# Optimization experiments

Measured on AMD Instinct MI355X. Metric: run time of the kernel, lower is better.

Reference implementation:

```python
import jax, jax.numpy as jnp
import numpy as np
from jax import lax

B, H, W = 256, 26, 4
LAT, QOUT = 64, 1024
K, D, Z = 4, 32, 64   # num_flows, num_ortho_vecs, z_size
STEPS = 100
BN_EPS = 1e-5


def setup_inputs():
    ks = iter(jax.random.split(jax.random.key(0), 80))
    def rn(shape, s=0.05):
        return jax.random.normal(next(ks), shape, jnp.float32) * s
    z1 = lambda n: jnp.zeros((n,), jnp.float32)
    o1 = lambda n: jnp.ones((n,), jnp.float32)
    return {
        "x": jax.random.normal(next(ks), (B, 1, H, W), jnp.float32),
        "eps": jax.random.normal(next(ks), (B, LAT), jnp.float32),
        "cw1": rn((32, 1, 3, 4)), "cb1": z1(32), "g1": o1(32), "be1": z1(32),
        "cw2": rn((16, 32, 5, 1)), "cb2": z1(16), "g2": o1(16), "be2": z1(16),
        "cw3": rn((8, 16, 7, 1)), "cb3": z1(8), "g3": o1(8), "be3": z1(8),
        "d1_w": rn((112, QOUT)), "d1_b": z1(QOUT), "bn1_g": o1(QOUT), "bn1_b": z1(QOUT),
        "mu_w": rn((QOUT, LAT)), "mu_b": z1(LAT),
        "lv_w": rn((QOUT, LAT)), "lv_b": z1(LAT),
        "ad_w": rn((QOUT, K * D * D)), "ad_b": z1(K * D * D),
        "adg1_w": rn((QOUT, K * D)), "adg1_b": z1(K * D),
        "adg2_w": rn((QOUT, K * D)), "adg2_b": z1(K * D),
        "aq_w": rn((QOUT, K * Z * D)), "aq_b": rn((K * Z * D,), 0.05),
        "ab_w": rn((QOUT, K * D)), "ab_b": z1(K * D),
        "d3_w": rn((LAT, QOUT)), "d3_b": z1(QOUT), "bn3_g": o1(QOUT), "bn3_b": z1(QOUT),
        "d4_w": rn((QOUT, 112)), "d4_b": z1(112), "bn4_g": o1(112), "bn4_b": z1(112),
        "tw1": rn((8, 16, 7, 1)), "tb1": z1(16), "tg1": o1(16), "tbe1": z1(16),
        "tw2": rn((16, 32, 5, 1)), "tb2": z1(32), "tg2": o1(32), "tbe2": z1(32),
        "tw3": rn((32, 1, 3, 4)), "tb3": z1(1),
    }


def _conv(x, w, b):
    y = lax.conv_general_dilated(x, w, (1, 1), 'VALID',
                                 dimension_numbers=('NCHW', 'OIHW', 'NCHW'))
    return y + b[None, :, None, None]


def _tconv(x, w, b):
    # torch ConvTranspose2d weight layout (in, out, kH, kW) == OIHW of the
    # forward conv being transposed -> transpose_kernel=True matches torch.
    y = lax.conv_transpose(x, w, (1, 1), 'VALID',
                           dimension_numbers=('NCHW', 'OIHW', 'NCHW'),
                           transpose_kernel=True)
    return y + b[None, :, None, None]


def _bn2d(x, g, b):  # BatchNorm2d, training mode (biased batch stats)
    m = x.mean((0, 2, 3), keepdims=True)
    v = ((x - m) ** 2).mean((0, 2, 3), keepdims=True)
    return (x - m) * lax.rsqrt(v + BN_EPS) * g[None, :, None, None] + b[None, :, None, None]


def _bn1d(x, g, b):  # BatchNorm1d, training mode
    m = x.mean(0)
    v = ((x - m) ** 2).mean(0)
    return (x - m) * lax.rsqrt(v + BN_EPS) * g + b


def reference(x, eps, cw1, cb1, g1, be1, cw2, cb2, g2, be2, cw3, cb3, g3, be3,
              d1_w, d1_b, bn1_g, bn1_b, mu_w, mu_b, lv_w, lv_b,
              ad_w, ad_b, adg1_w, adg1_b, adg2_w, adg2_b, aq_w, aq_b, ab_w, ab_b,
              d3_w, d3_b, bn3_g, bn3_b, d4_w, d4_b, bn4_g, bn4_b,
              tw1, tb1, tg1, tbe1, tw2, tb2, tg2, tbe2, tw3, tb3):
    # ---- encoder CNN ----
    h = jax.nn.relu(_bn2d(_conv(x, cw1, cb1), g1, be1))
    h = jax.nn.relu(_bn2d(_conv(h, cw2, cb2), g2, be2))
    h = jax.nn.relu(_bn2d(_conv(h, cw3, cb3), g3, be3))   # (B,8,14,1)
    out = h.reshape(B, -1)                                 # (B,112)
    out = jax.nn.relu(_bn1d(out @ d1_w + d1_b, bn1_g, bn1_b))
    mean = out @ mu_w + mu_b
    logvar = out @ lv_w + lv_b
    # ---- amortized flow parameters ----
    full_d = (out @ ad_w + ad_b).reshape(B, D, D, K)
    diag1 = jnp.tanh(out @ adg1_w + adg1_b).reshape(B, D, K)
    diag2 = jnp.tanh(out @ adg2_w + adg2_b).reshape(B, D, K)
    triu = jnp.triu(jnp.ones((D, D), x.dtype), 1)[None, :, :, None]
    di = jnp.arange(D)
    r1 = (full_d * triu).at[:, di, di, :].set(diag1)
    r2 = (jnp.transpose(full_d, (0, 2, 1, 3)) * triu).at[:, di, di, :].set(diag2)
    q = out @ aq_w + aq_b                                  # (B, K*Z*D)
    bflow = (out @ ab_w + ab_b).reshape(B, 1, D, K)
    # ---- Bjorck orthogonalization (100 fixed-point steps) ----
    qn = q.reshape(B * K, Z * D)
    qn = qn / jnp.linalg.norm(qn, axis=1, keepdims=True)
    amat = qn.reshape(B * K, Z, D)
    eye = jnp.eye(D, dtype=x.dtype)
    @jax.checkpoint
    def step(a, _):
        gram = jnp.einsum('nzd,nze->nde', a, a)            # a^T a, (N,D,D)
        a = jnp.einsum('nzd,nde->nze', a, eye + 0.5 * (eye - gram))
        return a, None
    amat, _ = lax.scan(step, amat, None, length=STEPS)
    q_ortho = amat.reshape(B, K, Z, D).transpose(1, 0, 2, 3)  # (K,B,Z,D)
    # ---- reparameterize + Sylvester flows ----
    z0 = mean + eps * jnp.exp(0.5 * logvar)
    z = z0
    ldj = jnp.zeros((B,), x.dtype)
    for k in range(K):
        r1k, r2k, qk, bk = r1[..., k], r2[..., k], q_ortho[k], bflow[..., k]
        qr2 = jnp.einsum('bzd,bed->bze', qk, r2k)          # q @ r2^T (B,Z,D)
        qr1 = jnp.einsum('bzd,bde->bze', qk, r1k)          # q @ r1   (B,Z,D)
        r2qzb = jnp.einsum('bz,bzd->bd', z, qr2)[:, None, :] + bk  # (B,1,D)
        z = jnp.einsum('bod,bzd->boz', jnp.tanh(r2qzb), qr1)[:, 0, :] + z
        dr1 = r1k[:, di, di]
        dr2 = r2k[:, di, di]
        diag_j = (1.0 - jnp.tanh(r2qzb) ** 2)[:, 0, :] * (dr1 * dr2) + 1.0
        ldj = ldj + jnp.log(jnp.abs(diag_j)).sum(-1)
    # ---- decoder ----
    d = jax.nn.relu(_bn1d(z @ d3_w + d3_b, bn3_g, bn3_b))
    d = jax.nn.relu(_bn1d(d @ d4_w + d4_b, bn4_g, bn4_b))
    d = d.reshape(B, 8, 14, 1)
    d = jax.nn.relu(_bn2d(_tconv(d, tw1, tb1), tg1, tbe1))
    d = jax.nn.relu(_bn2d(_tconv(d, tw2, tb2), tg2, tbe2))
    x_dec = _tconv(d, tw3, tb3)
    return (x_dec, mean, logvar, ldj, z0, z)
```

## Files before the change

kernel.cpp:

```cpp
#include <hip/hip_runtime.h>
#include <math.h>

#define NS_STEPS 30

typedef __attribute__((ext_vector_type(8))) _Float16 half8;
typedef __attribute__((ext_vector_type(4))) _Float16 half4v;
typedef __attribute__((ext_vector_type(8))) short short8;
typedef __attribute__((ext_vector_type(4))) float floatx4;

static __device__ inline unsigned short f2bf(float f) {
  union { float f; unsigned u; } v; v.f = f;
  unsigned r = v.u + 0x7fffu + ((v.u >> 16) & 1u);
  return (unsigned short)(r >> 16);
}
static __device__ inline float bf2f(unsigned short h) {
  union { unsigned u; float f; } v; v.u = ((unsigned)h) << 16;
  return v.f;
}

__global__ __launch_bounds__(256) void conv1_k(const float* __restrict__ x,
    const float* __restrict__ w, const float* __restrict__ bias,
    float* __restrict__ out) {
  __shared__ float ws[384];
  int tid = threadIdx.x;
  for (int i = tid; i < 384; i += 256) ws[i] = w[i];
  __syncthreads();
  int idx = blockIdx.x * 256 + tid;
  if (idx >= 196608) return;
  int b = idx / 768, r = idx % 768;
  int c = r / 24, h = r % 24;
  const float* xb = x + b * 104 + h * 4;
  const float* wc = ws + c * 12;
  float acc = bias[c];
  #pragma unroll
  for (int kh = 0; kh < 3; kh++) {
    #pragma unroll
    for (int kw = 0; kw < 4; kw++)
      acc += xb[kh * 4 + kw] * wc[kh * 4 + kw];
  }
  out[idx] = acc;
}

__global__ __launch_bounds__(256) void conv2_k(const float* __restrict__ in,
    const float* __restrict__ w, const float* __restrict__ bias,
    float* __restrict__ out) {
  __shared__ float ws[2560];
  int tid = threadIdx.x;
  for (int i = tid; i < 2560; i += 256) ws[i] = w[i];
  __syncthreads();
  int idx = blockIdx.x * 256 + tid;
  if (idx >= 81920) return;
  int b = idx / 320, r = idx % 320;
  int c = r / 20, h = r % 20;
  const float* ib = in + b * 768 + h;
  const float* wc = ws + c * 160;
  float acc = bias[c];
  for (int i = 0; i < 32; i++) {
    #pragma unroll
    for (int kh = 0; kh < 5; kh++)
      acc += ib[i * 24 + kh] * wc[i * 5 + kh];
  }
  out[idx] = acc;
}

__global__ __launch_bounds__(256) void conv3_k(const float* __restrict__ in,
    const float* __restrict__ w, const float* __restrict__ bias,
    float* __restrict__ out) {
  __shared__ float ws[896];
  int tid = threadIdx.x;
  for (int i = tid; i < 896; i += 256) ws[i] = w[i];
  __syncthreads();
  int idx = blockIdx.x * 256 + tid;
  if (idx >= 28672) return;
  int b = idx / 112, r = idx % 112;
  int c = r / 14, h = r % 14;
  const float* ib = in + b * 320 + h;
  const float* wc = ws + c * 112;
  float acc = bias[c];
  for (int i = 0; i < 16; i++) {
    #pragma unroll
    for (int kh = 0; kh < 7; kh++)
      acc += ib[i * 20 + kh] * wc[i * 7 + kh];
  }
  out[idx] = acc;
}

__global__ __launch_bounds__(256) void tconv1_k(const float* __restrict__ in,
    const float* __restrict__ w, const float* __restrict__ bias,
    float* __restrict__ out) {
  __shared__ float ws[896];
  int tid = threadIdx.x;
  for (int i = tid; i < 896; i += 256) ws[i] = w[i];
  __syncthreads();
  int idx = blockIdx.x * 256 + tid;
  if (idx >= 81920) return;
  int b = idx / 320, r = idx % 320;
  int c = r / 20, s = r % 20;
  float acc = bias[c];
  for (int o = 0; o < 8; o++) {
    #pragma unroll
    for (int kh = 0; kh < 7; kh++) {
      int hs = s - kh;
      if (hs >= 0 && hs < 14)
        acc += in[b * 112 + o * 14 + hs] * ws[o * 112 + c * 7 + kh];
    }
  }
  out[idx] = acc;
}

__global__ __launch_bounds__(256) void tconv2_k(const float* __restrict__ in,
    const float* __restrict__ w, const float* __restrict__ bias,
    float* __restrict__ out) {
  __shared__ float ws[2560];
  int tid = threadIdx.x;
  for (int i = tid; i < 2560; i += 256) ws[i] = w[i];
  __syncthreads();
  int idx = blockIdx.x * 256 + tid;
  if (idx >= 196608) return;
  int b = idx / 768, r = idx % 768;
  int c = r / 24, s = r % 24;
  float acc = bias[c];
  for (int o = 0; o < 16; o++) {
    #pragma unroll
    for (int kh = 0; kh < 5; kh++) {
      int hs = s - kh;
      if (hs >= 0 && hs < 20)
        acc += in[b * 320 + o * 20 + hs] * ws[o * 160 + c * 5 + kh];
    }
  }
  out[idx] = acc;
}

__global__ __launch_bounds__(256) void tconv3_k(const float* __restrict__ in,
    const float* __restrict__ w, const float* __restrict__ bias,
    float* __restrict__ out) {
  __shared__ float ws[384];
  int tid = threadIdx.x;
  for (int i = tid; i < 384; i += 256) ws[i] = w[i];
  __syncthreads();
  int idx = blockIdx.x * 256 + tid;
  if (idx >= 26624) return;
  int b = idx / 104, r = idx % 104;
  int sh = r / 4, sw = r % 4;
  float acc = bias[0];
  for (int o = 0; o < 32; o++) {
    #pragma unroll
    for (int kh = 0; kh < 3; kh++) {
      int hs = sh - kh;
      if (hs >= 0 && hs < 24)
        acc += in[b * 768 + o * 24 + hs] * ws[o * 12 + kh * 4 + sw];
    }
  }
  out[idx] = acc;
}

__global__ __launch_bounds__(256) void bn2d_k(float* __restrict__ x,
    const float* __restrict__ g, const float* __restrict__ be,
    int C, int HW) {
  __shared__ float rs[256], rs2[256];
  int c = blockIdx.x, tid = threadIdx.x;
  int total = 256 * HW;
  float s = 0.f, s2 = 0.f;
  for (int i = tid; i < total; i += 256) {
    int b = i / HW, j = i - b * HW;
    float v = x[(b * C + c) * HW + j];
    s += v; s2 += v * v;
  }
  rs[tid] = s; rs2[tid] = s2;
  __syncthreads();
  for (int off = 128; off > 0; off >>= 1) {
    if (tid < off) { rs[tid] += rs[tid + off]; rs2[tid] += rs2[tid + off]; }
    __syncthreads();
  }
  float m = rs[0] / (float)total;
  float var = rs2[0] / (float)total - m * m;
  float rstd = rsqrtf(var + 1e-5f) * g[c];
  float bb = be[c];
  for (int i = tid; i < total; i += 256) {
    int b = i / HW, j = i - b * HW;
    size_t idx = (size_t)(b * C + c) * HW + j;
    float v = (x[idx] - m) * rstd + bb;
    x[idx] = v > 0.f ? v : 0.f;
  }
}

__global__ __launch_bounds__(256) void bn1d_k(float* __restrict__ x,
    const float* __restrict__ g, const float* __restrict__ be, int N) {
  __shared__ float p1[8][32], p2[8][32];
  int t = threadIdx.x;
  int cl = t & 31, rg = t >> 5;
  int c = blockIdx.x * 32 + cl;
  float s = 0.f, s2 = 0.f;
  if (c < N) {
    for (int r = rg * 32; r < rg * 32 + 32; r++) {
      float v = x[r * N + c];
      s += v; s2 += v * v;
    }
  }
  p1[rg][cl] = s; p2[rg][cl] = s2;
  __syncthreads();
  float ts = 0.f, ts2 = 0.f;
  #pragma unroll
  for (int i = 0; i < 8; i++) { ts += p1[i][cl]; ts2 += p2[i][cl]; }
  float m = ts * (1.f / 256.f);
  float var = ts2 * (1.f / 256.f) - m * m;
  float rstd = rsqrtf(var + 1e-5f) * ((c < N) ? g[c] : 1.f);
  float bb = (c < N) ? be[c] : 0.f;
  if (c < N) {
    for (int r = rg * 32; r < rg * 32 + 32; r++) {
      float v = (x[r * N + c] - m) * rstd + bb;
      x[r * N + c] = v > 0.f ? v : 0.f;
    }
  }
}

__global__ __launch_bounds__(256) void gemm_os_k(const float* __restrict__ A,
    const float* __restrict__ W, const float* __restrict__ bias,
    float* __restrict__ C, int K, int N) {
  __shared__ float As[112 * 68];
  __shared__ float Bs[112 * 68];
  int tid = threadIdx.x;
  int nb = blockIdx.x, mb = blockIdx.y;
  int K16 = K >> 4;
  {
    int row = tid >> 2;
    const float* Ar = A + (size_t)(mb * 64 + row) * K;
    for (int i = 0; i < K16; i++) {
      int j = (tid & 3) + 4 * i;
      float4 v = *(const float4*)(Ar + j * 4);
      int k = j * 4;
      As[k * 68 + row] = v.x;
      As[(k + 1) * 68 + row] = v.y;
      As[(k + 2) * 68 + row] = v.z;
      As[(k + 3) * 68 + row] = v.w;
    }
  }
  {
    int n4 = (tid & 15) * 4;
    for (int i = 0; i < K16; i++) {
      int k = (tid >> 4) + 16 * i;
      float4 v = *(const float4*)(W + (size_t)k * N + nb * 64 + n4);
      *(float4*)(Bs + k * 68 + n4) = v;
    }
  }
  __syncthreads();
  int tm = tid >> 4, tn = tid & 15;
  int m0 = tm * 4, n0 = tn * 4;
  float acc[4][4] = {{0.f}};
  #pragma unroll 8
  for (int kk = 0; kk < K; kk++) {
    float4 a = *(const float4*)(As + kk * 68 + m0);
    float4 b = *(const float4*)(Bs + kk * 68 + n0);
    acc[0][0] += a.x*b.x; acc[0][1] += a.x*b.y; acc[0][2] += a.x*b.z; acc[0][3] += a.x*b.w;
    acc[1][0] += a.y*b.x; acc[1][1] += a.y*b.y; acc[1][2] += a.y*b.z; acc[1][3] += a.y*b.w;
    acc[2][0] += a.z*b.x; acc[2][1] += a.z*b.y; acc[2][2] += a.z*b.z; acc[2][3] += a.z*b.w;
    acc[3][0] += a.w*b.x; acc[3][1] += a.w*b.y; acc[3][2] += a.w*b.z; acc[3][3] += a.w*b.w;
  }
  #pragma unroll
  for (int i = 0; i < 4; i++) {
    int m = mb * 64 + m0 + i;
    #pragma unroll
    for (int j = 0; j < 4; j++) {
      int n = nb * 64 + n0 + j;
      C[(size_t)m * N + n] = acc[i][j] + bias[n];
    }
  }
}

__global__ __launch_bounds__(256) void gemm_ks_k(const float* __restrict__ A,
    const float* __restrict__ W, const float* __restrict__ bias,
    float* __restrict__ C) {
  __shared__ float As[64 * 68];
  __shared__ float Bs[64 * 68];
  int tid = threadIdx.x;
  int nb = blockIdx.x, mb = blockIdx.y, kc = blockIdx.z;
  int k0 = kc * 64;
  {
    int row = tid >> 2;
    const float* Ar = A + (size_t)(mb * 64 + row) * 1024 + k0;
    #pragma unroll
    for (int i = 0; i < 4; i++) {
      int j = (tid & 3) + 4 * i;
      float4 v = *(const float4*)(Ar + j * 4);
      int k = j * 4;
      As[k * 68 + row] = v.x;
      As[(k + 1) * 68 + row] = v.y;
      As[(k + 2) * 68 + row] = v.z;
      As[(k + 3) * 68 + row] = v.w;
    }
  }
  {
    int n4 = (tid & 15) * 4;
    int nbase = nb * 64 + n4;
    #pragma unroll
    for (int i = 0; i < 4; i++) {
      int k = (tid >> 4) + 16 * i;
      const float* Wr = W + (size_t)(k0 + k) * 112;
      float4 v;
      v.x = (nbase     < 112) ? Wr[nbase]     : 0.f;
      v.y = (nbase + 1 < 112) ? Wr[nbase + 1] : 0.f;
      v.z = (nbase + 2 < 112) ? Wr[nbase + 2] : 0.f;
      v.w = (nbase + 3 < 112) ? Wr[nbase + 3] : 0.f;
      *(float4*)(Bs + k * 68 + n4) = v;
    }
  }
  __syncthreads();
  int tm = tid >> 4, tn = tid & 15;
  int m0 = tm * 4, n0 = tn * 4;
  float acc[4][4] = {{0.f}};
  #pragma unroll 8
  for (int kk = 0; kk < 64; kk++) {
    float4 a = *(const float4*)(As + kk * 68 + m0);
    float4 b = *(const float4*)(Bs + kk * 68 + n0);
    acc[0][0] += a.x*b.x; acc[0][1] += a.x*b.y; acc[0][2] += a.x*b.z; acc[0][3] += a.x*b.w;
    acc[1][0] += a.y*b.x; acc[1][1] += a.y*b.y; acc[1][2] += a.y*b.z; acc[1][3] += a.y*b.w;
    acc[2][0] += a.z*b.x; acc[2][1] += a.z*b.y; acc[2][2] += a.z*b.z; acc[2][3] += a.z*b.w;
    acc[3][0] += a.w*b.x; acc[3][1] += a.w*b.y; acc[3][2] += a.w*b.z; acc[3][3] += a.w*b.w;
  }
  #pragma unroll
  for (int i = 0; i < 4; i++) {
    int m = mb * 64 + m0 + i;
    #pragma unroll
    for (int j = 0; j < 4; j++) {
      int n = nb * 64 + n0 + j;
      if (n < 112) {
        float v = acc[i][j] + (kc == 0 ? bias[n] : 0.f);
        atomicAdd(&C[m * 112 + n], v);
      }
    }
  }
}

__global__ __launch_bounds__(256) void prep_a_k(const float* __restrict__ A,
    short* __restrict__ ahi, short* __restrict__ alo) {
  int gi = blockIdx.x * 256 + threadIdx.x;
  int lane = gi & 63;
  int t = gi >> 6;
  int mt = t & 3; t >>= 2;
  int c = t & 31; int mb = t >> 5;
  int row = mb * 64 + mt * 16 + (lane & 15);
  int k0 = c * 32 + (lane >> 4) * 8;
  const float* src = A + (size_t)row * 1024 + k0;
  float4 v0 = *(const float4*)(src);
  float4 v1 = *(const float4*)(src + 4);
  float av[8] = {v0.x, v0.y, v0.z, v0.w, v1.x, v1.y, v1.z, v1.w};
  short8 h, lo;
  #pragma unroll
  for (int i = 0; i < 8; i++) {
    unsigned short hh = f2bf(av[i]);
    h[i] = (short)hh;
    lo[i] = (short)f2bf(av[i] - bf2f(hh));
  }
  *(short8*)(ahi + (size_t)gi * 8) = h;
  *(short8*)(alo + (size_t)gi * 8) = lo;
}

struct HeadArgs {
  const float* W[7];
  const float* b[7];
  float* dst[7];
  int off[8];
  int ldw[7];
  int op[7];
};

__global__ __launch_bounds__(256) void heads_mfma_k(const short* __restrict__ ahi,
                                                    const short* __restrict__ alo,
                                                    HeadArgs ha) {
  int tid = threadIdx.x;
  int nb = blockIdx.x;
  int gc = nb * 16;
  int r = 0;
  while (gc >= ha.off[r + 1]) r++;
  const float* Wp = ha.W[r];
  const float* bias = ha.b[r];
  float* dst = ha.dst[r];
  int ldw = ha.ldw[r];
  int op = ha.op[r];
  int nloc = gc - ha.off[r];

  int w = tid >> 6, l = tid & 63;
  int lane16 = l & 15, quad = l >> 4;

  const float* wptr = Wp + (size_t)(quad * 8) * ldw + nloc + lane16;
  const short* agh = ahi + (size_t)w * 65536;
  const short* agl = alo + (size_t)w * 65536;

  const floatx4 zero4 = {0.f, 0.f, 0.f, 0.f};
  floatx4 acc[4] = {zero4, zero4, zero4, zero4};

  float wvN[8], wvF[8];
  short8 whi, wlo;
  short8 aCh[4], aCl[4], aNh[4], aNl[4];

  {
    float wv0[8];
    #pragma unroll
    for (int j = 0; j < 8; j++) wv0[j] = wptr[(size_t)j * ldw];
    #pragma unroll
    for (int mt = 0; mt < 4; mt++) {
      size_t ao = (size_t)mt * 512 + l * 8;
      aCh[mt] = *(const short8*)(agh + ao);
      aCl[mt] = *(const short8*)(agl + ao);
    }
    #pragma unroll
    for (int j = 0; j < 8; j++) wvN[j] = wptr[(size_t)(32 + j) * ldw];
    #pragma unroll
    for (int j = 0; j < 8; j++) {
      unsigned short hh = f2bf(wv0[j]);
      whi[j] = (short)hh;
      wlo[j] = (short)f2bf(wv0[j] - bf2f(hh));
    }
  }

  for (int ch = 0; ch < 32; ++ch) {
    if (ch < 30) {
      #pragma unroll
      for (int j = 0; j < 8; j++)
        wvF[j] = wptr[(size_t)((ch + 2) * 32 + j) * ldw];
    }
    if (ch < 31) {
      #pragma unroll
      for (int mt = 0; mt < 4; mt++) {
        size_t ao = (size_t)((ch + 1) * 4 + mt) * 512 + l * 8;
        aNh[mt] = *(const short8*)(agh + ao);
        aNl[mt] = *(const short8*)(agl + ao);
      }
    }
    #pragma unroll
    for (int mt = 0; mt < 4; mt++) {
      acc[mt] = __builtin_amdgcn_mfma_f32_16x16x32_bf16(aCh[mt], whi, acc[mt], 0, 0, 0);
      acc[mt] = __builtin_amdgcn_mfma_f32_16x16x32_bf16(aCh[mt], wlo, acc[mt], 0, 0, 0);
      acc[mt] = __builtin_amdgcn_mfma_f32_16x16x32_bf16(aCl[mt], whi, acc[mt], 0, 0, 0);
    }
    if (ch < 31) {
      #pragma unroll
      for (int j = 0; j < 8; j++) {
        unsigned short hh = f2bf(wvN[j]);
        whi[j] = (short)hh;
        wlo[j] = (short)f2bf(wvN[j] - bf2f(hh));
      }
      #pragma unroll
      for (int mt = 0; mt < 4; mt++) { aCh[mt] = aNh[mt]; aCl[mt] = aNl[mt]; }
    }
    if (ch < 30) {
      #pragma unroll
      for (int j = 0; j < 8; j++) wvN[j] = wvF[j];
    }
  }

  int n = nloc + lane16;
  float bv = bias[n];
  #pragma unroll
  for (int mt = 0; mt < 4; mt++) {
    #pragma unroll
    for (int i = 0; i < 4; i++) {
      int m = w * 64 + mt * 16 + quad * 4 + i;
      float v = acc[mt][i] + bv;
      if (op == 1) v = tanhf(v);
      dst[(size_t)m * ldw + n] = v;
    }
  }
}

__global__ __launch_bounds__(128) void ns_f16split_k(const float* __restrict__ q,
                                                     float* __restrict__ amat) {
  __align__(16) __shared__ _Float16 arena[12288];
  int tid = threadIdx.x;
  int wid = tid >> 6;
  int l = tid & 63;
  int lane16 = l & 15, quad = l >> 4;
  _Float16* Ah_cm = arena;
  _Float16* Al_cm = arena + 2304;
  _Float16* Mh_cm = arena + 4608;
  _Float16* Ml_cm = arena + 5888;
  _Float16* Ah_rm = arena + 7168;
  _Float16* Al_rm = arena + 9728;
  float* Afin = (float*)arena;

  const float* g = q + (size_t)blockIdx.x * 2048;
  float* o = amat + (size_t)blockIdx.x * 2048;

  if (wid == 0) {
    float vals[32];
    float ss = 0.f;
    #pragma unroll
    for (int j = 0; j < 8; j++) {
      float4 v = *(const float4*)(g + l * 32 + j * 4);
      vals[4*j] = v.x; vals[4*j+1] = v.y; vals[4*j+2] = v.z; vals[4*j+3] = v.w;
      ss += v.x*v.x + v.y*v.y + v.z*v.z + v.w*v.w;
    }
    #pragma unroll
    for (int off = 32; off > 0; off >>= 1) ss += __shfl_xor(ss, off);
    float rn = rsqrtf(ss);
    #pragma unroll
    for (int i = 0; i < 32; i++) vals[i] *= rn;
    #pragma unroll
    for (int j = 0; j < 8; j++) {
      half4v ph, pl;
      #pragma unroll
      for (int rr = 0; rr < 4; rr++) {
        float v = vals[4*j + rr];
        _Float16 h = (_Float16)v;
        _Float16 lo = (_Float16)(v - (float)h);
        ph[rr] = h; pl[rr] = lo;
      }
      *(half4v*)(Ah_rm + l * 40 + j * 4) = ph;
      *(half4v*)(Al_rm + l * 40 + j * 4) = pl;
    }
    #pragma unroll
    for (int i = 0; i < 32; i++) {
      float v = vals[i];
      _Float16 h = (_Float16)v;
      Ah_cm[i * 72 + l] = h;
      Al_cm[i * 72 + l] = (_Float16)(v - (float)h);
    }
  }
  __syncthreads();

  const floatx4 zero4 = {0.f, 0.f, 0.f, 0.f};
  for (int s = 0; s < NS_STEPS; s++) {
    bool last = (s == NS_STEPS - 1);
    half8 fgh[2], fgl[2];
    #pragma unroll
    for (int c = 0; c < 2; c++) {
      fgh[c] = *(half8*)(Ah_cm + (wid * 16 + lane16) * 72 + c * 32 + quad * 8);
      fgl[c] = *(half8*)(Al_cm + (wid * 16 + lane16) * 72 + c * 32 + quad * 8);
    }
    half8 fah[2][2], fal[2][2];
    #pragma unroll
    for (int ti = 0; ti < 2; ti++)
      #pragma unroll
      for (int c = 0; c < 2; c++) {
        fah[ti][c] = *(half8*)(Ah_cm + (ti * 16 + lane16) * 72 + c * 32 + quad * 8);
        fal[ti][c] = *(half8*)(Al_cm + (ti * 16 + lane16) * 72 + c * 32 + quad * 8);
      }
    floatx4 gf[2] = {zero4, zero4};
    #pragma unroll
    for (int ti = 0; ti < 2; ti++)
      #pragma unroll
      for (int c = 0; c < 2; c++) {
        gf[ti] = __builtin_amdgcn_mfma_f32_16x16x32_f16(
            fah[ti][c], fgh[c], gf[ti], 0, 0, 0);
        gf[ti] = __builtin_amdgcn_mfma_f32_16x16x32_f16(
            fah[ti][c], fgl[c], gf[ti], 0, 0, 0);
        gf[ti] = __builtin_amdgcn_mfma_f32_16x16x32_f16(
            fal[ti][c], fgh[c], gf[ti], 0, 0, 0);
      }
    #pragma unroll
    for (int ti = 0; ti < 2; ti++) {
      int col = wid * 16 + lane16;
      int row0 = ti * 16 + quad * 4;
      half4v ph, pl;
      #pragma unroll
      for (int rr = 0; rr < 4; rr++) {
        float m = ((row0 + rr) == col ? 1.5f : 0.f) - 0.5f * gf[ti][rr];
        _Float16 h = (_Float16)m;
        ph[rr] = h; pl[rr] = (_Float16)(m - (float)h);
      }
      *(half4v*)(Mh_cm + col * 40 + row0) = ph;
      *(half4v*)(Ml_cm + col * 40 + row0) = pl;
    }
    __syncthreads();
    half8 fmh[2], fml[2], fbh[2], fbl[2];
    #pragma unroll
    for (int ti = 0; ti < 2; ti++) {
      fmh[ti] = *(half8*)(Mh_cm + (ti * 16 + lane16) * 40 + quad * 8);
      fml[ti] = *(half8*)(Ml_cm + (ti * 16 + lane16) * 40 + quad * 8);
    }
    #pragma unroll
    for (int jj = 0; jj < 2; jj++) {
      int tj = 2 * wid + jj;
      fbh[jj] = *(half8*)(Ah_rm + (tj * 16 + lane16) * 40 + quad * 8);
      fbl[jj] = *(half8*)(Al_rm + (tj * 16 + lane16) * 40 + quad * 8);
    }
    floatx4 df[2][2];
    #pragma unroll
    for (int ti = 0; ti < 2; ti++)
      #pragma unroll
      for (int jj = 0; jj < 2; jj++) {
        df[ti][jj] = __builtin_amdgcn_mfma_f32_16x16x32_f16(
            fmh[ti], fbh[jj], zero4, 0, 0, 0);
        df[ti][jj] = __builtin_amdgcn_mfma_f32_16x16x32_f16(
            fmh[ti], fbl[jj], df[ti][jj], 0, 0, 0);
        df[ti][jj] = __builtin_amdgcn_mfma_f32_16x16x32_f16(
            fml[ti], fbh[jj], df[ti][jj], 0, 0, 0);
      }
    __syncthreads();
    if (!last) {
      #pragma unroll
      for (int ti = 0; ti < 2; ti++)
        #pragma unroll
        for (int jj = 0; jj < 2; jj++) {
          int tj = 2 * wid + jj;
          int z = tj * 16 + lane16;
          int d0 = ti * 16 + quad * 4;
          half4v ph, pl;
          #pragma unroll
          for (int rr = 0; rr < 4; rr++) {
            float v = df[ti][jj][rr];
            _Float16 h = (_Float16)v;
            ph[rr] = h; pl[rr] = (_Float16)(v - (float)h);
          }
          *(half4v*)(Ah_rm + z * 40 + d0) = ph;
          *(half4v*)(Al_rm + z * 40 + d0) = pl;
          #pragma unroll
          for (int rr = 0; rr < 4; rr++) {
            Ah_cm[(d0 + rr) * 72 + z] = ph[rr];
            Al_cm[(d0 + rr) * 72 + z] = pl[rr];
          }
        }
    } else {
      #pragma unroll
      for (int ti = 0; ti < 2; ti++)
        #pragma unroll
        for (int jj = 0; jj < 2; jj++) {
          int tj = 2 * wid + jj;
          int z = tj * 16 + lane16;
          int d0 = ti * 16 + quad * 4;
          float4 v;
          v.x = df[ti][jj][0]; v.y = df[ti][jj][1];
          v.z = df[ti][jj][2]; v.w = df[ti][jj][3];
          *(float4*)(Afin + z * 36 + d0) = v;
        }
    }
    __syncthreads();
  }
  #pragma unroll
  for (int j = 0; j < 4; j++) {
    int f = j * 512 + tid * 4;
    int z = f >> 5, d = f & 31;
    float4 v = *(const float4*)(Afin + z * 36 + d);
    *(float4*)(o + f) = v;
  }
}

__global__ __launch_bounds__(64) void flow_k(const float* __restrict__ amat,
    const float* __restrict__ fd, const float* __restrict__ dg1,
    const float* __restrict__ dg2, const float* __restrict__ ab,
    const float* __restrict__ eps, float* __restrict__ dout) {
  __shared__ float Ps[32][64];
  __shared__ float wsh[32], tsh[32], ush[32];
  int b = blockIdx.x, l = threadIdx.x;
  float mv  = dout[26624 + b * 64 + l];
  float lvv = dout[43008 + b * 64 + l];
  float z0 = mv + eps[b * 64 + l] * expf(0.5f * lvv);
  dout[59648 + b * 64 + l] = z0;
  float zv = z0;
  float ldj = 0.f;
  float q[32];
  for (int k = 0; k < 4; k++) {
    const float4* qrow = (const float4*)(amat + (size_t)(b * 4 + k) * 2048 + l * 32);
    #pragma unroll
    for (int j = 0; j < 8; j++) {
      float4 v = qrow[j];
      q[4*j] = v.x; q[4*j+1] = v.y; q[4*j+2] = v.z; q[4*j+3] = v.w;
    }
    #pragma unroll
    for (int d = 0; d < 32; d++) Ps[d][l] = zv * q[d];
    __syncthreads();
    if (l < 32) {
      const float4* pr = (const float4*)Ps[l];
      float s = 0.f;
      #pragma unroll
      for (int j = 0; j < 16; j++) {
        float4 v = pr[j];
        s += v.x + v.y + v.z + v.w;
      }
      wsh[l] = s;
    }
    __syncthreads();
    if (l < 32) {
      int e = l;
      float acc = ab[b * 128 + e * 4 + k] + wsh[e] * dg2[b * 128 + e * 4 + k];
      for (int d = e + 1; d < 32; d++)
        acc += wsh[d] * fd[b * 4096 + d * 128 + e * 4 + k];
      float tt = tanhf(acc);
      tsh[e] = tt;
      float dd = (1.f - tt * tt) * (dg1[b*128 + e*4 + k] * dg2[b*128 + e*4 + k]) + 1.f;
      ldj += logf(fabsf(dd));
    }
    __syncthreads();
    if (l < 32) {
      int d = l;
      float acc = tsh[d] * dg1[b * 128 + d * 4 + k];
      for (int e = d + 1; e < 32; e++)
        acc += fd[b * 4096 + d * 128 + e * 4 + k] * tsh[e];
      ush[d] = acc;
    }
    __syncthreads();
    #pragma unroll
    for (int d = 0; d < 32; d++) zv += q[d] * ush[d];
    __syncthreads();
  }
  dout[76032 + b * 64 + l] = zv;
  for (int off = 16; off > 0; off >>= 1) ldj += __shfl_down(ldj, off, 32);
  if (l == 0) dout[59392 + b] = ldj;
}

extern "C" void kernel_launch(void* const* d_in, const int* in_sizes, int n_in,
                              void* d_out, int out_size, void* d_ws, size_t ws_size,
                              hipStream_t stream) {
  (void)in_sizes; (void)n_in; (void)out_size; (void)ws_size;
  const float* x     = (const float*)d_in[0];
  const float* eps   = (const float*)d_in[1];
  const float* cw1   = (const float*)d_in[2];
  const float* cb1   = (const float*)d_in[3];
  const float* g1    = (const float*)d_in[4];
  const float* be1   = (const float*)d_in[5];
  const float* cw2   = (const float*)d_in[6];
  const float* cb2   = (const float*)d_in[7];
  const float* g2    = (const float*)d_in[8];
  const float* be2   = (const float*)d_in[9];
  const float* cw3   = (const float*)d_in[10];
  const float* cb3   = (const float*)d_in[11];
  const float* g3    = (const float*)d_in[12];
  const float* be3   = (const float*)d_in[13];
  const float* d1_w  = (const float*)d_in[14];
  const float* d1_b  = (const float*)d_in[15];
  const float* bn1_g = (const float*)d_in[16];
  const float* bn1_b = (const float*)d_in[17];
  const float* mu_w  = (const float*)d_in[18];
  const float* mu_b  = (const float*)d_in[19];
  const float* lv_w  = (const float*)d_in[20];
  const float* lv_b  = (const float*)d_in[21];
  const float* ad_w  = (const float*)d_in[22];
  const float* ad_b  = (const float*)d_in[23];
  const float* adg1_w= (const float*)d_in[24];
  const float* adg1_b= (const float*)d_in[25];
  const float* adg2_w= (const float*)d_in[26];
  const float* adg2_b= (const float*)d_in[27];
  const float* aq_w  = (const float*)d_in[28];
  const float* aq_b  = (const float*)d_in[29];
  const float* ab_w  = (const float*)d_in[30];
  const float* ab_b  = (const float*)d_in[31];
  const float* d3_w  = (const float*)d_in[32];
  const float* d3_b  = (const float*)d_in[33];
  const float* bn3_g = (const float*)d_in[34];
  const float* bn3_b = (const float*)d_in[35];
  const float* d4_w  = (const float*)d_in[36];
  const float* d4_b  = (const float*)d_in[37];
  const float* bn4_g = (const float*)d_in[38];
  const float* bn4_b = (const float*)d_in[39];
  const float* tw1   = (const float*)d_in[40];
  const float* tb1   = (const float*)d_in[41];
  const float* tg1   = (const float*)d_in[42];
  const float* tbe1  = (const float*)d_in[43];
  const float* tw2   = (const float*)d_in[44];
  const float* tb2   = (const float*)d_in[45];
  const float* tg2   = (const float*)d_in[46];
  const float* tbe2  = (const float*)d_in[47];
  const float* tw3   = (const float*)d_in[48];
  const float* tb3   = (const float*)d_in[49];

  float* out = (float*)d_out;
  float* wsf = (float*)d_ws;
  float* h1   = wsf;
  float* h2   = wsf + 196608;
  float* h3   = wsf + 278528;
  float* out1 = wsf + 307200;
  float* fd   = wsf + 569344;
  float* dg1  = wsf + 1617920;
  float* dg2  = wsf + 1650688;
  float* qb   = wsf + 1683456;
  float* ab   = wsf + 3780608;
  float* amat = wsf + 3813376;
  float* dec1 = out1;
  float* dec2 = h3;
  float* t1   = h2;
  float* t2   = h1;

  short* ahi = (short*)wsf;
  short* alo = ahi + 262144;

  float* mean_o = out + 26624;
  float* lv_o   = out + 43008;
  float* z_o    = out + 76032;

  conv1_k<<<768, 256, 0, stream>>>(x, cw1, cb1, h1);
  bn2d_k<<<32, 256, 0, stream>>>(h1, g1, be1, 32, 24);
  conv2_k<<<320, 256, 0, stream>>>(h1, cw2, cb2, h2);
  bn2d_k<<<16, 256, 0, stream>>>(h2, g2, be2, 16, 20);
  conv3_k<<<112, 256, 0, stream>>>(h2, cw3, cb3, h3);
  bn2d_k<<<8, 256, 0, stream>>>(h3, g3, be3, 8, 14);

  gemm_os_k<<<dim3(16, 4), 256, 0, stream>>>(h3, d1_w, d1_b, out1, 112, 1024);
  bn1d_k<<<32, 256, 0, stream>>>(out1, bn1_g, bn1_b, 1024);

  prep_a_k<<<128, 256, 0, stream>>>(out1, ahi, alo);

  HeadArgs ha;
  ha.W[0] = mu_w;   ha.b[0] = mu_b;   ha.dst[0] = mean_o; ha.ldw[0] = 64;   ha.op[0] = 0;
  ha.W[1] = lv_w;   ha.b[1] = lv_b;   ha.dst[1] = lv_o;   ha.ldw[1] = 64;   ha.op[1] = 0;
  ha.W[2] = ad_w;   ha.b[2] = ad_b;   ha.dst[2] = fd;     ha.ldw[2] = 4096; ha.op[2] = 0;
  ha.W[3] = adg1_w; ha.b[3] = adg1_b; ha.dst[3] = dg1;    ha.ldw[3] = 128;  ha.op[3] = 1;
  ha.W[4] = adg2_w; ha.b[4] = adg2_b; ha.dst[4] = dg2;    ha.ldw[4] = 128;  ha.op[4] = 1;
  ha.W[5] = aq_w;   ha.b[5] = aq_b;   ha.dst[5] = qb;     ha.ldw[5] = 8192; ha.op[5] = 0;
  ha.W[6] = ab_w;   ha.b[6] = ab_b;   ha.dst[6] = ab;     ha.ldw[6] = 128;  ha.op[6] = 0;
  ha.off[0] = 0;    ha.off[1] = 64;   ha.off[2] = 128;  ha.off[3] = 4224;
  ha.off[4] = 4352; ha.off[5] = 4480; ha.off[6] = 12672; ha.off[7] = 12800;
  heads_mfma_k<<<dim3(800), 256, 0, stream>>>(ahi, alo, ha);

  ns_f16split_k<<<1024, 128, 0, stream>>>(qb, amat);
  flow_k<<<256, 64, 0, stream>>>(amat, fd, dg1, dg2, ab, eps, out);

  gemm_os_k<<<dim3(16, 4), 256, 0, stream>>>(z_o, d3_w, d3_b, dec1, 64, 1024);
  bn1d_k<<<32, 256, 0, stream>>>(dec1, bn3_g, bn3_b, 1024);
  hipMemsetAsync(dec2, 0, 28672 * sizeof(float), stream);
  gemm_ks_k<<<dim3(2, 4, 16), 256, 0, stream>>>(dec1, d4_w, d4_b, dec2);
  bn1d_k<<<4, 256, 0, stream>>>(dec2, bn4_g, bn4_b, 112);

  tconv1_k<<<320, 256, 0, stream>>>(dec2, tw1, tb1, t1);
  bn2d_k<<<16, 256, 0, stream>>>(t1, tg1, tbe1, 16, 20);
  tconv2_k<<<768, 256, 0, stream>>>(t1, tw2, tb2, t2);
  bn2d_k<<<32, 256, 0, stream>>>(t2, tg2, tbe2, 32, 24);
  tconv3_k<<<104, 256, 0, stream>>>(t2, tw3, tb3, out);
}
```

Measured before the change: 531.1 us.

## Retile heads GEMM to 64-column blocks with LDS-shared split-bf16 weights

The heads MFMA kernel is retiled so each block covers 64 output columns and a 64-row quarter of the batch, instead of 16 columns by all 256 rows. The grid changes from 800 blocks to 200x4. Each thread loads one weight column slice, splits it into bf16 hi/lo parts, and stores them in a double-buffered LDS tile that all four waves read, with a barrier per K chunk. This cuts redundant weight loads and conversions and raises the loads per thread, but it adds LDS traffic, a barrier every iteration, and reloads of the A operand across the four row blocks.

```diff
diff --git a/kernel.cpp b/kernel.cpp
--- a/kernel.cpp
+++ b/kernel.cpp
@@ -367,9 +367,11 @@
 __global__ __launch_bounds__(256) void heads_mfma_k(const short* __restrict__ ahi,
                                                     const short* __restrict__ alo,
                                                     HeadArgs ha) {
+  __shared__ __align__(16) short Wsh[2][2][2048];
   int tid = threadIdx.x;
   int nb = blockIdx.x;
-  int gc = nb * 16;
+  int mq = blockIdx.y;
+  int gc = nb * 64;
   int r = 0;
   while (gc >= ha.off[r + 1]) r++;
   const float* Wp = ha.W[r];
@@ -382,81 +384,111 @@
   int w = tid >> 6, l = tid & 63;
   int lane16 = l & 15, quad = l >> 4;
 
-  const float* wptr = Wp + (size_t)(quad * 8) * ldw + nloc + lane16;
-  const short* agh = ahi + (size_t)w * 65536;
-  const short* agl = alo + (size_t)w * 65536;
+  int c64 = tid & 63, q4 = tid >> 6;
+  const float* wcol = Wp + (size_t)(q4 * 8) * ldw + nloc + c64;
+  int wg = ((c64 >> 4) * 64 + q4 * 16 + (c64 & 15)) * 8;
+
+  const short* agh = ahi + (size_t)mq * 65536 + w * 512 + l * 8;
+  const short* agl = alo + (size_t)mq * 65536 + w * 512 + l * 8;
 
   const floatx4 zero4 = {0.f, 0.f, 0.f, 0.f};
   floatx4 acc[4] = {zero4, zero4, zero4, zero4};
 
   float wvN[8], wvF[8];
-  short8 whi, wlo;
-  short8 aCh[4], aCl[4], aNh[4], aNl[4];
+  short8 whiN, wloN;
+  short8 aCh, aCl, aNh, aNl;
 
   {
     float wv0[8];
     #pragma unroll
-    for (int j = 0; j < 8; j++) wv0[j] = wptr[(size_t)j * ldw];
-    #pragma unroll
-    for (int mt = 0; mt < 4; mt++) {
-      size_t ao = (size_t)mt * 512 + l * 8;
-      aCh[mt] = *(const short8*)(agh + ao);
-      aCl[mt] = *(const short8*)(agl + ao);
-    }
-    #pragma unroll
-    for (int j = 0; j < 8; j++) wvN[j] = wptr[(size_t)(32 + j) * ldw];
+    for (int j = 0; j < 8; j++) wv0[j] = wcol[(size_t)j * ldw];
+    #pragma unroll
+    for (int j = 0; j < 8; j++) wvN[j] = wcol[(size_t)(32 + j) * ldw];
+    aCh = *(const short8*)(agh);
+    aCl = *(const short8*)(agl);
+    #pragma unroll
+    for (int j = 0; j < 8; j++) wvF[j] = wcol[(size_t)(64 + j) * ldw];
+    short8 t0h, t0l;
     #pragma unroll
     for (int j = 0; j < 8; j++) {
       unsigned short hh = f2bf(wv0[j]);
-      whi[j] = (short)hh;
-      wlo[j] = (short)f2bf(wv0[j] - bf2f(hh));
-    }
+      t0h[j] = (short)hh;
+      t0l[j] = (short)f2bf(wv0[j] - bf2f(hh));
+    }
+    *(short8*)(&Wsh[0][0][wg]) = t0h;
+    *(short8*)(&Wsh[0][1][wg]) = t0l;
+    #pragma unroll
+    for (int j = 0; j < 8; j++) {
+      unsigned short hh = f2bf(wvN[j]);
+      whiN[j] = (short)hh;
+      wloN[j] = (short)f2bf(wvN[j] - bf2f(hh));
+    }
+    #pragma unroll
+    for (int j = 0; j < 8; j++) wvN[j] = wvF[j];
+    asm volatile("s_waitcnt lgkmcnt(0)" ::: "memory");
+    __builtin_amdgcn_s_barrier();
   }
 
   for (int ch = 0; ch < 32; ++ch) {
+    int p = ch & 1;
+    if (ch < 31) {
+      *(short8*)(&Wsh[p ^ 1][0][wg]) = whiN;
+      *(short8*)(&Wsh[p ^ 1][1][wg]) = wloN;
+    }
+    if (ch < 29) {
+      #pragma unroll
+      for (int j = 0; j < 8; j++)
+        wvF[j] = wcol[(size_t)((ch + 3) * 32 + j) * ldw];
+    }
+    if (ch < 31) {
+      aNh = *(const short8*)(agh + (size_t)(ch + 1) * 2048);
+      aNl = *(const short8*)(agl + (size_t)(ch + 1) * 2048);
+    }
+    short8 bh0 = *(const short8*)(&Wsh[p][0][(0 * 64 + l) * 8]);
+    short8 bl0 = *(const short8*)(&Wsh[p][1][(0 * 64 + l) * 8]);
+    short8 bh1 = *(const short8*)(&Wsh[p][0][(1 * 64 + l) * 8]);
+    short8 bl1 = *(const short8*)(&Wsh[p][1][(1 * 64 + l) * 8]);
+    short8 bh2 = *(const short8*)(&Wsh[p][0][(2 * 64 + l) * 8]);
+    short8 bl2 = *(const short8*)(&Wsh[p][1][(2 * 64 + l) * 8]);
+    short8 bh3 = *(const short8*)(&Wsh[p][0][(3 * 64 + l) * 8]);
+    short8 bl3 = *(const short8*)(&Wsh[p][1][(3 * 64 + l) * 8]);
+    acc[0] = __builtin_amdgcn_mfma_f32_16x16x32_bf16(aCh, bh0, acc[0], 0, 0, 0);
+    acc[0] = __builtin_amdgcn_mfma_f32_16x16x32_bf16(aCh, bl0, acc[0], 0, 0, 0);
+    acc[0] = __builtin_amdgcn_mfma_f32_16x16x32_bf16(aCl, bh0, acc[0], 0, 0, 0);
+    acc[1] = __builtin_amdgcn_mfma_f32_16x16x32_bf16(aCh, bh1, acc[1], 0, 0, 0);
+    acc[1] = __builtin_amdgcn_mfma_f32_16x16x32_bf16(aCh, bl1, acc[1], 0, 0, 0);
+    acc[1] = __builtin_amdgcn_mfma_f32_16x16x32_bf16(aCl, bh1, acc[1], 0, 0, 0);
+    acc[2] = __builtin_amdgcn_mfma_f32_16x16x32_bf16(aCh, bh2, acc[2], 0, 0, 0);
+    acc[2] = __builtin_amdgcn_mfma_f32_16x16x32_bf16(aCh, bl2, acc[2], 0, 0, 0);
+    acc[2] = __builtin_amdgcn_mfma_f32_16x16x32_bf16(aCl, bh2, acc[2], 0, 0, 0);
+    acc[3] = __builtin_amdgcn_mfma_f32_16x16x32_bf16(aCh, bh3, acc[3], 0, 0, 0);
+    acc[3] = __builtin_amdgcn_mfma_f32_16x16x32_bf16(aCh, bl3, acc[3], 0, 0, 0);
+    acc[3] = __builtin_amdgcn_mfma_f32_16x16x32_bf16(aCl, bh3, acc[3], 0, 0, 0);
     if (ch < 30) {
-      #pragma unroll
-      for (int j = 0; j < 8; j++)
-        wvF[j] = wptr[(size_t)((ch + 2) * 32 + j) * ldw];
-    }
-    if (ch < 31) {
-      #pragma unroll
-      for (int mt = 0; mt < 4; mt++) {
-        size_t ao = (size_t)((ch + 1) * 4 + mt) * 512 + l * 8;
-        aNh[mt] = *(const short8*)(agh + ao);
-        aNl[mt] = *(const short8*)(agl + ao);
-      }
-    }
-    #pragma unroll
-    for (int mt = 0; mt < 4; mt++) {
-      acc[mt] = __builtin_amdgcn_mfma_f32_16x16x32_bf16(aCh[mt], whi, acc[mt], 0, 0, 0);
-      acc[mt] = __builtin_amdgcn_mfma_f32_16x16x32_bf16(aCh[mt], wlo, acc[mt], 0, 0, 0);
-      acc[mt] = __builtin_amdgcn_mfma_f32_16x16x32_bf16(aCl[mt], whi, acc[mt], 0, 0, 0);
-    }
-    if (ch < 31) {
       #pragma unroll
       for (int j = 0; j < 8; j++) {
         unsigned short hh = f2bf(wvN[j]);
-        whi[j] = (short)hh;
-        wlo[j] = (short)f2bf(wvN[j] - bf2f(hh));
+        whiN[j] = (short)hh;
+        wloN[j] = (short)f2bf(wvN[j] - bf2f(hh));
       }
-      #pragma unroll
-      for (int mt = 0; mt < 4; mt++) { aCh[mt] = aNh[mt]; aCl[mt] = aNl[mt]; }
-    }
-    if (ch < 30) {
+    }
+    if (ch < 29) {
       #pragma unroll
       for (int j = 0; j < 8; j++) wvN[j] = wvF[j];
     }
-  }
-
-  int n = nloc + lane16;
-  float bv = bias[n];
+    if (ch < 31) { aCh = aNh; aCl = aNl; }
+    asm volatile("s_waitcnt lgkmcnt(0)" ::: "memory");
+    __builtin_amdgcn_s_barrier();
+  }
+
   #pragma unroll
-  for (int mt = 0; mt < 4; mt++) {
+  for (int nf = 0; nf < 4; nf++) {
+    int n = nloc + nf * 16 + lane16;
+    float bv = bias[n];
     #pragma unroll
     for (int i = 0; i < 4; i++) {
-      int m = w * 64 + mt * 16 + quad * 4 + i;
-      float v = acc[mt][i] + bv;
+      int m = mq * 64 + w * 16 + quad * 4 + i;
+      float v = acc[nf][i] + bv;
       if (op == 1) v = tanhf(v);
       dst[(size_t)m * ldw + n] = v;
     }
@@ -799,7 +831,7 @@
   ha.W[6] = ab_w;   ha.b[6] = ab_b;   ha.dst[6] = ab;     ha.ldw[6] = 128;  ha.op[6] = 0;
   ha.off[0] = 0;    ha.off[1] = 64;   ha.off[2] = 128;  ha.off[3] = 4224;
   ha.off[4] = 4352; ha.off[5] = 4480; ha.off[6] = 12672; ha.off[7] = 12800;
-  heads_mfma_k<<<dim3(800), 256, 0, stream>>>(ahi, alo, ha);
+  heads_mfma_k<<<dim3(200, 4), 256, 0, stream>>>(ahi, alo, ha);
 
   ns_f16split_k<<<1024, 128, 0, stream>>>(qb, amat);
   flow_k<<<256, 64, 0, stream>>>(amat, fd, dg1, dg2, ab, eps, out);
```

New measurement: 510.1 us, median of 2. -3.9%, faster.
